# Kernel optimization log

Measured on AMD Instinct MI355X. Metric: run time of the kernel, lower is better.

Reference implementation:

```python
import jax, jax.numpy as jnp
import numpy as np

L1 = 0.05
L2 = 0.05
L3 = 0.05
L4 = 0.05
D_MIN = 1.0
EPS = 1e-12


def _pairwise_dist(x, y):
    sq = (jnp.sum(x * x, axis=-1)[:, None]
          + jnp.sum(y * y, axis=-1)[None, :]
          - 2.0 * (x @ y.T))
    return jnp.sqrt(jnp.clip(sq, EPS))


def setup_inputs() -> dict:
    key = jax.random.key(0)
    k1, k2, k3, k4, k5, k6 = jax.random.split(key, 6)
    B, C, D, d, P = 32768, 100, 1024, 512, 128
    return {
        "predictions": jax.random.normal(k1, (B, C), dtype=jnp.float32),
        "reconstructions": jax.random.normal(k2, (B, D), dtype=jnp.float32),
        "data": jax.random.normal(k3, (B, D), dtype=jnp.float32),
        "embeddings": jax.random.normal(k4, (B, d), dtype=jnp.float32),
        "prototypes": jax.random.normal(k5, (P, d), dtype=jnp.float32),
        "labels": jax.random.randint(k6, (B,), 0, C, dtype=jnp.int64),
    }


def reference(predictions, reconstructions, data, embeddings, prototypes, labels):
    B = predictions.shape[0]
    P = prototypes.shape[0]

    # Cross-entropy (mean reduction, class-index targets)
    logp = jax.nn.log_softmax(predictions, axis=-1)
    classification_loss = -jnp.mean(logp[jnp.arange(B), labels])

    # MSE reconstruction loss (mean reduction)
    reconstruction_loss = jnp.mean((reconstructions - data) ** 2)

    # Prototype diversity penalty: sum_{j<k} max(0, d_min - ||p_j - p_k||)^2
    proto_dist = _pairwise_dist(prototypes, prototypes)  # [P, P]
    hinge = jnp.maximum(0.0, D_MIN - proto_dist) ** 2
    upper = jnp.triu(jnp.ones((P, P), dtype=bool), k=1)
    diversity_penalty = jnp.sum(jnp.where(upper, hinge, 0.0))

    # Embedding-to-prototype distances [B, P], shared by similarity/coverage penalties
    dist = _pairwise_dist(embeddings, prototypes)
    similarity_penalty = jnp.sum(jnp.min(dist, axis=0)) / P
    coverage_penalty = jnp.sum(jnp.min(dist, axis=1)) / B

    total_loss = (classification_loss
                  + L1 * reconstruction_loss
                  + L2 * diversity_penalty
                  + L3 * similarity_penalty
                  + L4 * coverage_penalty)
    return total_loss
```

## Files before the change

### kernel.cpp

```cpp
#include <hip/hip_runtime.h>
#include <hip/hip_bf16.h>


constexpr float FEPS = 1e-12f;
constexpr float DMIN = 1.0f;

#define NB_DIST 512
#define NB_MSE  1024
#define NB_CE   256
#define NB_DIV  128

typedef unsigned short ushort_t;
typedef __attribute__((ext_vector_type(8))) short bf16x8;
typedef __attribute__((ext_vector_type(8))) unsigned short u16x8;
typedef __attribute__((ext_vector_type(4))) unsigned short u16x4;
typedef __attribute__((ext_vector_type(16))) float f32x16;
typedef __attribute__((ext_vector_type(4))) float f32x4;

__device__ __forceinline__ unsigned short f2b(float f) {
    unsigned u = __float_as_uint(f);
    u += 0x7FFFu + ((u >> 16) & 1u);
    return (unsigned short)(u >> 16);
}

union SmemU {
    struct {
        char     As[8192];
        char     Bs[16384];
        float    rown[64];
        float    pn[128];
        unsigned rowmin[64];
        unsigned colmin[128];
    } dist;
    struct { float pp[512]; float spp; float sred[4]; } div;
    struct { float sred[4]; } red;
};

__global__ __launch_bounds__(128) void conv_kernel(const float* __restrict__ proto,
                                                   ushort_t* __restrict__ pB,
                                                   float* __restrict__ pnorm,
                                                   float* __restrict__ ws,
                                                   unsigned* __restrict__ proto_min) {
    int p = blockIdx.x, q = threadIdx.x;
    if (q == 0) proto_min[p] = 0x7F7F7F7Fu;
    if (p == 0 && q < 4) ws[q] = 0.f;
    float4 v = ((const float4*)(proto + (size_t)p * 512))[q];
    u16x4 o = { f2b(v.x), f2b(v.y), f2b(v.z), f2b(v.w) };
    *(u16x4*)(pB + (size_t)p * 512 + q * 4) = o;
    float s = v.x * v.x + v.y * v.y + v.z * v.z + v.w * v.w;
    #pragma unroll
    for (int off = 32; off; off >>= 1) s += __shfl_xor(s, off);
    __shared__ float sr[2];
    if ((q & 63) == 0) sr[q >> 6] = s;
    __syncthreads();
    if (q == 0) pnorm[p] = sr[0] + sr[1];
}

template<bool PRECONV>
__device__ __forceinline__ void dist_body(SmemU& sm, int bid,
                                          const float* __restrict__ emb,
                                          const float* __restrict__ proto,
                                          const ushort_t* __restrict__ pB,
                                          const float* __restrict__ pnormG,
                                          unsigned* __restrict__ proto_min,
                                          float* __restrict__ cov_out) {
    char*     AsB     = sm.dist.As;
    char*     BsB     = sm.dist.Bs;
    float*    rownL   = sm.dist.rown;
    float*    pnL     = sm.dist.pn;
    unsigned* rowminL = sm.dist.rowmin;
    unsigned* colminL = sm.dist.colmin;

    const int t  = threadIdx.x;
    const int m0 = bid * 64;

    if (t < 64)  { rownL[t] = 0.f; rowminL[t] = 0x7F7F7F7Fu; }
    if (t < 128) { colminL[t] = 0x7F7F7F7Fu; pnL[t] = PRECONV ? pnormG[t] : 0.f; }
    __syncthreads();

    const int ra = t >> 2, qa = t & 3;
    const int pb = t >> 1, hb = t & 1;
    const int raz = ra & 7, pbz = pb & 7;

    const float4* aG  = (const float4*)(emb + (size_t)(m0 + ra) * 512 + qa * 16);
    const u16x8*  bG  = (const u16x8*)(pB) + (size_t)pb * 64 + hb * 4;
    const float4* bGf = (const float4*)(proto + (size_t)pb * 512 + hb * 32);

    const int lane = t & 63, wv = t >> 6;
    const int wr = wv >> 1, wc = wv & 1;
    const int lo = lane & 31, hi = lane >> 5;
    const int arow = wr * 32 + lo;
    const int arz  = arow & 7;
    const int p0 = wc * 64 + lo, p1 = p0 + 32;
    const int pz = p0 & 7;

    float4 av0 = aG[0], av1 = aG[1], av2 = aG[2], av3 = aG[3];
    u16x8  bv0, bv1, bv2, bv3;
    float4 bf0, bf1, bf2, bf3, bf4, bf5, bf6, bf7;
    if constexpr (PRECONV) { bv0 = bG[0]; bv1 = bG[1]; bv2 = bG[2]; bv3 = bG[3]; }
    else { bf0 = bGf[0]; bf1 = bGf[1]; bf2 = bGf[2]; bf3 = bGf[3];
           bf4 = bGf[4]; bf5 = bGf[5]; bf6 = bGf[6]; bf7 = bGf[7]; }

    f32x16 acc0 = {}, acc1 = {};

    char* Aw = AsB + ra * 128;
    char* Bw = BsB + pb * 128;
    const char* Ar  = AsB + arow * 128;
    const char* Br0 = BsB + p0 * 128;
    const char* Br1 = BsB + p1 * 128;

    for (int c = 0; c < 8; ++c) {
        {
            float nx = 0.f;
            nx = fmaf(av0.x, av0.x, nx); nx = fmaf(av0.y, av0.y, nx);
            nx = fmaf(av0.z, av0.z, nx); nx = fmaf(av0.w, av0.w, nx);
            nx = fmaf(av1.x, av1.x, nx); nx = fmaf(av1.y, av1.y, nx);
            nx = fmaf(av1.z, av1.z, nx); nx = fmaf(av1.w, av1.w, nx);
            nx = fmaf(av2.x, av2.x, nx); nx = fmaf(av2.y, av2.y, nx);
            nx = fmaf(av2.z, av2.z, nx); nx = fmaf(av2.w, av2.w, nx);
            nx = fmaf(av3.x, av3.x, nx); nx = fmaf(av3.y, av3.y, nx);
            nx = fmaf(av3.z, av3.z, nx); nx = fmaf(av3.w, av3.w, nx);
            atomicAdd(&rownL[ra], nx);
            u16x8 w0 = { f2b(av0.x), f2b(av0.y), f2b(av0.z), f2b(av0.w),
                         f2b(av1.x), f2b(av1.y), f2b(av1.z), f2b(av1.w) };
            u16x8 w1 = { f2b(av2.x), f2b(av2.y), f2b(av2.z), f2b(av2.w),
                         f2b(av3.x), f2b(av3.y), f2b(av3.z), f2b(av3.w) };
            *(u16x8*)(Aw + (((qa * 2 + 0) ^ raz) << 4)) = w0;
            *(u16x8*)(Aw + (((qa * 2 + 1) ^ raz) << 4)) = w1;

            if constexpr (PRECONV) {
                *(u16x8*)(Bw + (((hb * 4 + 0) ^ pbz) << 4)) = bv0;
                *(u16x8*)(Bw + (((hb * 4 + 1) ^ pbz) << 4)) = bv1;
                *(u16x8*)(Bw + (((hb * 4 + 2) ^ pbz) << 4)) = bv2;
                *(u16x8*)(Bw + (((hb * 4 + 3) ^ pbz) << 4)) = bv3;
            } else {
                float pns = 0.f;
                pns = fmaf(bf0.x, bf0.x, pns); pns = fmaf(bf0.y, bf0.y, pns);
                pns = fmaf(bf0.z, bf0.z, pns); pns = fmaf(bf0.w, bf0.w, pns);
                pns = fmaf(bf1.x, bf1.x, pns); pns = fmaf(bf1.y, bf1.y, pns);
                pns = fmaf(bf1.z, bf1.z, pns); pns = fmaf(bf1.w, bf1.w, pns);
                pns = fmaf(bf2.x, bf2.x, pns); pns = fmaf(bf2.y, bf2.y, pns);
                pns = fmaf(bf2.z, bf2.z, pns); pns = fmaf(bf2.w, bf2.w, pns);
                pns = fmaf(bf3.x, bf3.x, pns); pns = fmaf(bf3.y, bf3.y, pns);
                pns = fmaf(bf3.z, bf3.z, pns); pns = fmaf(bf3.w, bf3.w, pns);
                pns = fmaf(bf4.x, bf4.x, pns); pns = fmaf(bf4.y, bf4.y, pns);
                pns = fmaf(bf4.z, bf4.z, pns); pns = fmaf(bf4.w, bf4.w, pns);
                pns = fmaf(bf5.x, bf5.x, pns); pns = fmaf(bf5.y, bf5.y, pns);
                pns = fmaf(bf5.z, bf5.z, pns); pns = fmaf(bf5.w, bf5.w, pns);
                pns = fmaf(bf6.x, bf6.x, pns); pns = fmaf(bf6.y, bf6.y, pns);
                pns = fmaf(bf6.z, bf6.z, pns); pns = fmaf(bf6.w, bf6.w, pns);
                pns = fmaf(bf7.x, bf7.x, pns); pns = fmaf(bf7.y, bf7.y, pns);
                pns = fmaf(bf7.z, bf7.z, pns); pns = fmaf(bf7.w, bf7.w, pns);
                atomicAdd(&pnL[pb], pns);
                u16x8 x0 = { f2b(bf0.x), f2b(bf0.y), f2b(bf0.z), f2b(bf0.w),
                             f2b(bf1.x), f2b(bf1.y), f2b(bf1.z), f2b(bf1.w) };
                u16x8 x1 = { f2b(bf2.x), f2b(bf2.y), f2b(bf2.z), f2b(bf2.w),
                             f2b(bf3.x), f2b(bf3.y), f2b(bf3.z), f2b(bf3.w) };
                u16x8 x2 = { f2b(bf4.x), f2b(bf4.y), f2b(bf4.z), f2b(bf4.w),
                             f2b(bf5.x), f2b(bf5.y), f2b(bf5.z), f2b(bf5.w) };
                u16x8 x3 = { f2b(bf6.x), f2b(bf6.y), f2b(bf6.z), f2b(bf6.w),
                             f2b(bf7.x), f2b(bf7.y), f2b(bf7.z), f2b(bf7.w) };
                *(u16x8*)(Bw + (((hb * 4 + 0) ^ pbz) << 4)) = x0;
                *(u16x8*)(Bw + (((hb * 4 + 1) ^ pbz) << 4)) = x1;
                *(u16x8*)(Bw + (((hb * 4 + 2) ^ pbz) << 4)) = x2;
                *(u16x8*)(Bw + (((hb * 4 + 3) ^ pbz) << 4)) = x3;
            }
        }
        __syncthreads();
        if (c < 7) {
            av0 = aG[(c + 1) * 16 + 0]; av1 = aG[(c + 1) * 16 + 1];
            av2 = aG[(c + 1) * 16 + 2]; av3 = aG[(c + 1) * 16 + 3];
            if constexpr (PRECONV) {
                bv0 = bG[(c + 1) * 8 + 0]; bv1 = bG[(c + 1) * 8 + 1];
                bv2 = bG[(c + 1) * 8 + 2]; bv3 = bG[(c + 1) * 8 + 3];
            } else {
                bf0 = bGf[(c + 1) * 16 + 0]; bf1 = bGf[(c + 1) * 16 + 1];
                bf2 = bGf[(c + 1) * 16 + 2]; bf3 = bGf[(c + 1) * 16 + 3];
                bf4 = bGf[(c + 1) * 16 + 4]; bf5 = bGf[(c + 1) * 16 + 5];
                bf6 = bGf[(c + 1) * 16 + 6]; bf7 = bGf[(c + 1) * 16 + 7];
            }
        }
        #pragma unroll
        for (int s = 0; s < 4; ++s) {
            const int g = (s * 2 + hi);
            bf16x8 af = *(const bf16x8*)(Ar  + ((g ^ arz) << 4));
            bf16x8 b0 = *(const bf16x8*)(Br0 + ((g ^ pz)  << 4));
            bf16x8 b1 = *(const bf16x8*)(Br1 + ((g ^ pz)  << 4));
            acc0 = __builtin_amdgcn_mfma_f32_32x32x16_bf16(af, b0, acc0, 0, 0, 0);
            acc1 = __builtin_amdgcn_mfma_f32_32x32x16_bf16(af, b1, acc1, 0, 0, 0);
        }
        __syncthreads();
    }

    const float pn0 = pnL[p0], pn1 = pnL[p1];
    float cmin0 = 3.0e38f, cmin1 = 3.0e38f;
    #pragma unroll
    for (int r = 0; r < 16; ++r) {
        const int row = wr * 32 + (r & 3) + 8 * (r >> 2) + 4 * hi;
        const float nx = rownL[row];
        float d0 = sqrtf(fmaxf(nx + pn0 - 2.f * acc0[r], FEPS));
        float d1 = sqrtf(fmaxf(nx + pn1 - 2.f * acc1[r], FEPS));
        cmin0 = fminf(cmin0, d0);
        cmin1 = fminf(cmin1, d1);
        atomicMin(&rowminL[row], __float_as_uint(fminf(d0, d1)));
    }
    atomicMin(&colminL[p0], __float_as_uint(cmin0));
    atomicMin(&colminL[p1], __float_as_uint(cmin1));
    __syncthreads();

    if (t < 64) {
        float cv = __uint_as_float(rowminL[t]);
        #pragma unroll
        for (int o = 32; o; o >>= 1) cv += __shfl_xor(cv, o);
        if (t == 0) atomicAdd(cov_out, cv);
    }
    if (t < 128) atomicMin(&proto_min[t], colminL[t]);
}

__device__ __forceinline__ void mse_body(SmemU& sm, int mb,
                                         const float4* __restrict__ r,
                                         const float4* __restrict__ d,
                                         float* __restrict__ out, int n4) {
    const int t  = threadIdx.x;
    const int CH = (n4 + NB_MSE - 1) / NB_MSE;
    const int base = mb * CH;
    const int L = (base + CH <= n4) ? CH : (n4 - base);
    const f32x4* rb = (const f32x4*)(r + base);
    const f32x4* db = (const f32x4*)(d + base);
    float acc0 = 0.f, acc1 = 0.f, acc2 = 0.f, acc3 = 0.f;
    int k = t;
    for (; k + 7 * 256 < L; k += 8 * 256) {
        f32x4 a0 = __builtin_nontemporal_load(&rb[k + 0 * 256]);
        f32x4 a1 = __builtin_nontemporal_load(&rb[k + 1 * 256]);
        f32x4 a2 = __builtin_nontemporal_load(&rb[k + 2 * 256]);
        f32x4 a3 = __builtin_nontemporal_load(&rb[k + 3 * 256]);
        f32x4 a4 = __builtin_nontemporal_load(&rb[k + 4 * 256]);
        f32x4 a5 = __builtin_nontemporal_load(&rb[k + 5 * 256]);
        f32x4 a6 = __builtin_nontemporal_load(&rb[k + 6 * 256]);
        f32x4 a7 = __builtin_nontemporal_load(&rb[k + 7 * 256]);
        f32x4 b0 = __builtin_nontemporal_load(&db[k + 0 * 256]);
        f32x4 b1 = __builtin_nontemporal_load(&db[k + 1 * 256]);
        f32x4 b2 = __builtin_nontemporal_load(&db[k + 2 * 256]);
        f32x4 b3 = __builtin_nontemporal_load(&db[k + 3 * 256]);
        f32x4 b4 = __builtin_nontemporal_load(&db[k + 4 * 256]);
        f32x4 b5 = __builtin_nontemporal_load(&db[k + 5 * 256]);
        f32x4 b6 = __builtin_nontemporal_load(&db[k + 6 * 256]);
        f32x4 b7 = __builtin_nontemporal_load(&db[k + 7 * 256]);
        f32x4 e;
        e = a0 - b0; acc0 = fmaf(e.x, e.x, acc0); acc1 = fmaf(e.y, e.y, acc1);
                     acc2 = fmaf(e.z, e.z, acc2); acc3 = fmaf(e.w, e.w, acc3);
        e = a1 - b1; acc0 = fmaf(e.x, e.x, acc0); acc1 = fmaf(e.y, e.y, acc1);
                     acc2 = fmaf(e.z, e.z, acc2); acc3 = fmaf(e.w, e.w, acc3);
        e = a2 - b2; acc0 = fmaf(e.x, e.x, acc0); acc1 = fmaf(e.y, e.y, acc1);
                     acc2 = fmaf(e.z, e.z, acc2); acc3 = fmaf(e.w, e.w, acc3);
        e = a3 - b3; acc0 = fmaf(e.x, e.x, acc0); acc1 = fmaf(e.y, e.y, acc1);
                     acc2 = fmaf(e.z, e.z, acc2); acc3 = fmaf(e.w, e.w, acc3);
        e = a4 - b4; acc0 = fmaf(e.x, e.x, acc0); acc1 = fmaf(e.y, e.y, acc1);
                     acc2 = fmaf(e.z, e.z, acc2); acc3 = fmaf(e.w, e.w, acc3);
        e = a5 - b5; acc0 = fmaf(e.x, e.x, acc0); acc1 = fmaf(e.y, e.y, acc1);
                     acc2 = fmaf(e.z, e.z, acc2); acc3 = fmaf(e.w, e.w, acc3);
        e = a6 - b6; acc0 = fmaf(e.x, e.x, acc0); acc1 = fmaf(e.y, e.y, acc1);
                     acc2 = fmaf(e.z, e.z, acc2); acc3 = fmaf(e.w, e.w, acc3);
        e = a7 - b7; acc0 = fmaf(e.x, e.x, acc0); acc1 = fmaf(e.y, e.y, acc1);
                     acc2 = fmaf(e.z, e.z, acc2); acc3 = fmaf(e.w, e.w, acc3);
    }
    for (; k < L; k += 256) {
        f32x4 a = __builtin_nontemporal_load(&rb[k]);
        f32x4 b = __builtin_nontemporal_load(&db[k]);
        f32x4 e = a - b;
        acc0 = fmaf(e.x, e.x, acc0); acc1 = fmaf(e.y, e.y, acc1);
        acc2 = fmaf(e.z, e.z, acc2); acc3 = fmaf(e.w, e.w, acc3);
    }
    float acc = (acc0 + acc1) + (acc2 + acc3);
    #pragma unroll
    for (int o = 32; o; o >>= 1) acc += __shfl_xor(acc, o);
    int lane = t & 63, w = t >> 6;
    if (lane == 0) sm.red.sred[w] = acc;
    __syncthreads();
    if (t == 0) atomicAdd(out, sm.red.sred[0] + sm.red.sred[1]
                             + sm.red.sred[2] + sm.red.sred[3]);
}

__device__ __forceinline__ void ce_body(SmemU& sm, int cb,
                                        const float* __restrict__ pred,
                                        const int* __restrict__ lab,
                                        float* __restrict__ ce_out,
                                        int B, int C) {
    const int rows_per_wave = B / (NB_CE * 4);
    int lane = threadIdx.x & 63;
    int w    = threadIdx.x >> 6;
    int wid  = cb * 4 + w;
    float acc = 0.f;
    for (int i = 0; i < rows_per_wave; ++i) {
        int row = wid * rows_per_wave + i;
        const float* p = pred + (size_t)row * C;
        float v1 = (lane < C)      ? p[lane]      : -3.0e38f;
        float v2 = (lane + 64 < C) ? p[lane + 64] : -3.0e38f;
        float m = fmaxf(v1, v2);
        #pragma unroll
        for (int o = 32; o; o >>= 1) m = fmaxf(m, __shfl_xor(m, o));
        float s = ((lane < C) ? __expf(v1 - m) : 0.f)
                + ((lane + 64 < C) ? __expf(v2 - m) : 0.f);
        #pragma unroll
        for (int o = 32; o; o >>= 1) s += __shfl_xor(s, o);
        float lv = p[lab[row]];
        acc += m + __logf(s) - lv;
    }
    if (lane == 0) sm.red.sred[w] = acc;
    __syncthreads();
    if (threadIdx.x == 0) atomicAdd(ce_out, sm.red.sred[0] + sm.red.sred[1]
                                          + sm.red.sred[2] + sm.red.sred[3]);
}

__device__ __forceinline__ void div_body(SmemU& sm, int p,
                                         const float* __restrict__ proto,
                                         float* __restrict__ div_out, int dd) {
    int q = threadIdx.x;
    bool act = q < 128;
    if (act) for (int k = q; k < dd; k += 128) sm.div.pp[k] = proto[(size_t)p * dd + k];
    __syncthreads();
    float dot = 0.f, qq = 0.f;
    if (act) {
        const float4* pq4 = (const float4*)(proto + (size_t)q * dd);
        const float4* pp4 = (const float4*)sm.div.pp;
        for (int k4 = 0; k4 < dd / 4; ++k4) {
            float4 v = pq4[k4];
            float4 u = pp4[k4];
            dot = fmaf(u.x, v.x, dot); dot = fmaf(u.y, v.y, dot);
            dot = fmaf(u.z, v.z, dot); dot = fmaf(u.w, v.w, dot);
            qq  = fmaf(v.x, v.x, qq);  qq  = fmaf(v.y, v.y, qq);
            qq  = fmaf(v.z, v.z, qq);  qq  = fmaf(v.w, v.w, qq);
        }
        if (q == p) sm.div.spp = qq;
    }
    __syncthreads();
    float h2 = 0.f;
    if (act && q > p) {
        float sq = sm.div.spp + qq - 2.f * dot;
        float dist = sqrtf(fmaxf(sq, FEPS));
        float h = fmaxf(0.f, DMIN - dist);
        h2 = h * h;
    }
    #pragma unroll
    for (int o = 32; o; o >>= 1) h2 += __shfl_xor(h2, o);
    if ((q & 63) == 0) sm.div.sred[q >> 6] = h2;
    __syncthreads();
    if (q == 0) atomicAdd(div_out, sm.div.sred[0] + sm.div.sred[1]
                                 + sm.div.sred[2] + sm.div.sred[3]);
}

template<bool PRECONV>
__global__ __launch_bounds__(256) void fused_kernel(
        const float* __restrict__ pred, const int* __restrict__ lab,
        const float4* __restrict__ recon4, const float4* __restrict__ data4,
        const float* __restrict__ emb, const float* __restrict__ proto,
        const ushort_t* __restrict__ pB, const float* __restrict__ pnormG,
        float* __restrict__ ws, unsigned* __restrict__ proto_min,
        int B, int C, int n4, int dd) {
    __shared__ __attribute__((aligned(16))) SmemU sm;
    int bid = blockIdx.x;
    if (bid < NB_DIST) {
        dist_body<PRECONV>(sm, bid, emb, proto, pB, pnormG, proto_min, ws + 3);
    } else if (bid < NB_DIST + NB_MSE) {
        mse_body(sm, bid - NB_DIST, recon4, data4, ws + 1, n4);
    } else if (bid < NB_DIST + NB_MSE + NB_CE) {
        ce_body(sm, bid - NB_DIST - NB_MSE, pred, lab, ws + 0, B, C);
    } else {
        div_body(sm, bid - NB_DIST - NB_MSE - NB_CE, proto, ws + 2, dd);
    }
}

__global__ void final_kernel(const float* __restrict__ ws,
                             const unsigned* __restrict__ pmin,
                             float* __restrict__ out, int B, int D, int P) {
    float sim = 0.f;
    for (int i = 0; i < P; ++i) sim += __uint_as_float(pmin[i]);
    float ce  = ws[0] / (float)B;
    float mse = ws[1] / ((float)B * (float)D);
    out[0] = ce + 0.05f * mse + 0.05f * ws[2] + 0.05f * (sim / (float)P)
           + 0.05f * (ws[3] / (float)B);
}

extern "C" void kernel_launch(void* const* d_in, const int* in_sizes, int n_in,
                              void* d_out, int out_size, void* d_ws, size_t ws_size,
                              hipStream_t stream) {
    const float* pred  = (const float*)d_in[0];
    const float* recon = (const float*)d_in[1];
    const float* data  = (const float*)d_in[2];
    const float* emb   = (const float*)d_in[3];
    const float* proto = (const float*)d_in[4];
    const int*   lab   = (const int*)d_in[5];
    float* out = (float*)d_out;

    int B  = in_sizes[5];
    int C  = in_sizes[0] / B;
    int D  = in_sizes[1] / B;
    int dd = in_sizes[3] / B;
    int P  = in_sizes[4] / dd;

    float* ws = (float*)d_ws;
    unsigned* proto_min = (unsigned*)(ws + 4);
    float*    pnorm     = ws + 132;
    ushort_t* pB        = (ushort_t*)((char*)d_ws + 1280);
    bool preconv = ws_size >= (size_t)(1280 + 128 * 512 * 2);

    int n4 = (B * D) / 4;
    int grid = NB_DIST + NB_MSE + NB_CE + NB_DIV;
    if (preconv) {
        conv_kernel<<<128, 128, 0, stream>>>(proto, pB, pnorm, ws, proto_min);
        fused_kernel<true><<<grid, 256, 0, stream>>>(
            pred, lab, (const float4*)recon, (const float4*)data, emb, proto,
            pB, pnorm, ws, proto_min, B, C, n4, dd);
    } else {
        hipMemsetAsync(ws, 0, 4 * sizeof(float), stream);
        hipMemsetAsync(ws + 4, 0x7F, P * sizeof(unsigned), stream);
        fused_kernel<false><<<grid, 256, 0, stream>>>(
            pred, lab, (const float4*)recon, (const float4*)data, emb, proto,
            nullptr, nullptr, ws, proto_min, B, C, n4, dd);
    }
    final_kernel<<<1, 1, 0, stream>>>(ws, proto_min, out, B, D, P);
}
```

Baseline: 105.9 us.

## Pipeline distance GEMM with direct global-to-LDS prototype loads and register double-buffering

The preconverted distance path now loads bf16 prototype tiles straight into LDS with global_load_lds, pre-swizzling the source addresses. Embedding loads are double-buffered in registers with the next chunk prefetched before the current one is converted. Row-norm atomics are collapsed to one per thread at the end, and explicit waitcnt and barriers replace __syncthreads. Launch bounds now request 4 blocks per CU. This aims to hide memory latency and remove the register round-trip for B, at the risk of fragile hand-written waitcnt ordering and extra register pressure.

```diff
diff --git a/kernel.cpp b/kernel.cpp
--- a/kernel.cpp
+++ b/kernel.cpp
@@ -16,6 +16,9 @@
 typedef __attribute__((ext_vector_type(4))) unsigned short u16x4;
 typedef __attribute__((ext_vector_type(16))) float f32x16;
 typedef __attribute__((ext_vector_type(4))) float f32x4;
+
+typedef __attribute__((address_space(1))) const void gvoid_t;
+typedef __attribute__((address_space(3))) void lvoid_t;
 
 __device__ __forceinline__ unsigned short f2b(float f) {
     unsigned u = __float_as_uint(f);
@@ -56,14 +59,12 @@
     if (q == 0) pnorm[p] = sr[0] + sr[1];
 }
 
-template<bool PRECONV>
-__device__ __forceinline__ void dist_body(SmemU& sm, int bid,
-                                          const float* __restrict__ emb,
-                                          const float* __restrict__ proto,
-                                          const ushort_t* __restrict__ pB,
-                                          const float* __restrict__ pnormG,
-                                          unsigned* __restrict__ proto_min,
-                                          float* __restrict__ cov_out) {
+__device__ __forceinline__ void dist_body_fast(SmemU& sm, int bid,
+                                               const float* __restrict__ emb,
+                                               const ushort_t* __restrict__ pB,
+                                               const float* __restrict__ pnormG,
+                                               unsigned* __restrict__ proto_min,
+                                               float* __restrict__ cov_out) {
     char*     AsB     = sm.dist.As;
     char*     BsB     = sm.dist.Bs;
     float*    rownL   = sm.dist.rown;
@@ -75,16 +76,28 @@
     const int m0 = bid * 64;
 
     if (t < 64)  { rownL[t] = 0.f; rowminL[t] = 0x7F7F7F7Fu; }
-    if (t < 128) { colminL[t] = 0x7F7F7F7Fu; pnL[t] = PRECONV ? pnormG[t] : 0.f; }
-    __syncthreads();
-
-    const int ra = t >> 2, qa = t & 3;
-    const int pb = t >> 1, hb = t & 1;
-    const int raz = ra & 7, pbz = pb & 7;
-
-    const float4* aG  = (const float4*)(emb + (size_t)(m0 + ra) * 512 + qa * 16);
-    const u16x8*  bG  = (const u16x8*)(pB) + (size_t)pb * 64 + hb * 4;
-    const float4* bGf = (const float4*)(proto + (size_t)pb * 512 + hb * 32);
+    if (t < 128) { colminL[t] = 0x7F7F7F7Fu; pnL[t] = pnormG[t]; }
+
+    int aidx[4], rowi[4], swzi[4];
+    const float4* embF4 = (const float4*)emb;
+    #pragma unroll
+    for (int i = 0; i < 4; ++i) {
+        int flat = i * 256 + t;
+        int row = flat >> 4, colq = flat & 15;
+        rowi[i] = row;
+        aidx[i] = (m0 + row) * 128 + colq;
+        swzi[i] = row * 128 + ((((colq >> 1) ^ (row & 7)) << 4) | ((colq & 1) << 3));
+    }
+
+    const ushort_t* bsrcp[4];
+    char* bdstW[4];
+    #pragma unroll
+    for (int i = 0; i < 4; ++i) {
+        int f = i * 256 + t;
+        int pr = f >> 3, gb = f & 7;
+        bsrcp[i] = pB + pr * 512 + ((gb ^ (pr & 7)) << 3);
+        bdstW[i] = BsB + (size_t)(i * 256 + (t & ~63)) * 16;
+    }
 
     const int lane = t & 63, wv = t >> 6;
     const int wr = wv >> 1, wc = wv & 1;
@@ -93,16 +106,146 @@
     const int arz  = arow & 7;
     const int p0 = wc * 64 + lo, p1 = p0 + 32;
     const int pz = p0 & 7;
+    const char* Ar  = AsB + arow * 128;
+    const char* Br0 = BsB + p0 * 128;
+    const char* Br1 = BsB + p1 * 128;
+
+    float4 aE0 = embF4[aidx[0]], aE1 = embF4[aidx[1]],
+           aE2 = embF4[aidx[2]], aE3 = embF4[aidx[3]];
+    float4 aO0, aO1, aO2, aO3;
+    float rn0 = 0.f, rn1 = 0.f, rn2 = 0.f, rn3 = 0.f;
+    f32x16 acc0 = {}, acc1 = {};
+    __syncthreads();
+
+#define DIST_CHUNK(c, W0, W1, W2, W3, L0, L1, L2, L3)                          \
+    {                                                                          \
+        const int kc = (c) * 64;                                               \
+        __builtin_amdgcn_global_load_lds((gvoid_t*)(bsrcp[0] + kc),            \
+                                         (lvoid_t*)bdstW[0], 16, 0, 0);        \
+        __builtin_amdgcn_global_load_lds((gvoid_t*)(bsrcp[1] + kc),            \
+                                         (lvoid_t*)bdstW[1], 16, 0, 0);        \
+        __builtin_amdgcn_global_load_lds((gvoid_t*)(bsrcp[2] + kc),            \
+                                         (lvoid_t*)bdstW[2], 16, 0, 0);        \
+        __builtin_amdgcn_global_load_lds((gvoid_t*)(bsrcp[3] + kc),            \
+                                         (lvoid_t*)bdstW[3], 16, 0, 0);        \
+        __builtin_amdgcn_sched_barrier(0);                                     \
+        {                                                                      \
+            const int kn = ((c) < 7 ? (c) + 1 : 7) * 16;                       \
+            L0 = embF4[aidx[0] + kn]; L1 = embF4[aidx[1] + kn];                \
+            L2 = embF4[aidx[2] + kn]; L3 = embF4[aidx[3] + kn];                \
+        }                                                                      \
+        __builtin_amdgcn_sched_barrier(0);                                     \
+        rn0 = fmaf(W0.x, W0.x, rn0); rn0 = fmaf(W0.y, W0.y, rn0);              \
+        rn0 = fmaf(W0.z, W0.z, rn0); rn0 = fmaf(W0.w, W0.w, rn0);              \
+        rn1 = fmaf(W1.x, W1.x, rn1); rn1 = fmaf(W1.y, W1.y, rn1);              \
+        rn1 = fmaf(W1.z, W1.z, rn1); rn1 = fmaf(W1.w, W1.w, rn1);              \
+        rn2 = fmaf(W2.x, W2.x, rn2); rn2 = fmaf(W2.y, W2.y, rn2);              \
+        rn2 = fmaf(W2.z, W2.z, rn2); rn2 = fmaf(W2.w, W2.w, rn2);              \
+        rn3 = fmaf(W3.x, W3.x, rn3); rn3 = fmaf(W3.y, W3.y, rn3);              \
+        rn3 = fmaf(W3.z, W3.z, rn3); rn3 = fmaf(W3.w, W3.w, rn3);              \
+        { u16x4 u = { f2b(W0.x), f2b(W0.y), f2b(W0.z), f2b(W0.w) };            \
+          *(u16x4*)(AsB + swzi[0]) = u; }                                      \
+        { u16x4 u = { f2b(W1.x), f2b(W1.y), f2b(W1.z), f2b(W1.w) };            \
+          *(u16x4*)(AsB + swzi[1]) = u; }                                      \
+        { u16x4 u = { f2b(W2.x), f2b(W2.y), f2b(W2.z), f2b(W2.w) };            \
+          *(u16x4*)(AsB + swzi[2]) = u; }                                      \
+        { u16x4 u = { f2b(W3.x), f2b(W3.y), f2b(W3.z), f2b(W3.w) };            \
+          *(u16x4*)(AsB + swzi[3]) = u; }                                      \
+        asm volatile("s_waitcnt vmcnt(4)" ::: "memory");                       \
+        asm volatile("s_waitcnt lgkmcnt(0)" ::: "memory");                     \
+        __builtin_amdgcn_s_barrier();                                          \
+        __builtin_amdgcn_sched_barrier(0);                                     \
+        _Pragma("unroll")                                                      \
+        for (int s = 0; s < 4; ++s) {                                          \
+            const int g = (s * 2 + hi);                                        \
+            bf16x8 af = *(const bf16x8*)(Ar  + ((g ^ arz) << 4));              \
+            bf16x8 b0 = *(const bf16x8*)(Br0 + ((g ^ pz)  << 4));              \
+            bf16x8 b1 = *(const bf16x8*)(Br1 + ((g ^ pz)  << 4));              \
+            acc0 = __builtin_amdgcn_mfma_f32_32x32x16_bf16(af, b0, acc0, 0,0,0); \
+            acc1 = __builtin_amdgcn_mfma_f32_32x32x16_bf16(af, b1, acc1, 0,0,0); \
+        }                                                                      \
+        asm volatile("s_waitcnt lgkmcnt(0)" ::: "memory");                     \
+        __builtin_amdgcn_s_barrier();                                          \
+        __builtin_amdgcn_sched_barrier(0);                                     \
+    }
+
+    #pragma unroll
+    for (int c = 0; c < 8; c += 2) {
+        DIST_CHUNK(c,     aE0, aE1, aE2, aE3, aO0, aO1, aO2, aO3)
+        DIST_CHUNK(c + 1, aO0, aO1, aO2, aO3, aE0, aE1, aE2, aE3)
+    }
+#undef DIST_CHUNK
+
+    atomicAdd(&rownL[rowi[0]], rn0);
+    atomicAdd(&rownL[rowi[1]], rn1);
+    atomicAdd(&rownL[rowi[2]], rn2);
+    atomicAdd(&rownL[rowi[3]], rn3);
+    __syncthreads();
+
+    const float pn0 = pnL[p0], pn1 = pnL[p1];
+    float cmin0 = 3.0e38f, cmin1 = 3.0e38f;
+    #pragma unroll
+    for (int r = 0; r < 16; ++r) {
+        const int row = wr * 32 + (r & 3) + 8 * (r >> 2) + 4 * hi;
+        const float nx = rownL[row];
+        float d0 = sqrtf(fmaxf(nx + pn0 - 2.f * acc0[r], FEPS));
+        float d1 = sqrtf(fmaxf(nx + pn1 - 2.f * acc1[r], FEPS));
+        cmin0 = fminf(cmin0, d0);
+        cmin1 = fminf(cmin1, d1);
+        atomicMin(&rowminL[row], __float_as_uint(fminf(d0, d1)));
+    }
+    atomicMin(&colminL[p0], __float_as_uint(cmin0));
+    atomicMin(&colminL[p1], __float_as_uint(cmin1));
+    __syncthreads();
+
+    if (t < 64) {
+        float cv = __uint_as_float(rowminL[t]);
+        #pragma unroll
+        for (int o = 32; o; o >>= 1) cv += __shfl_xor(cv, o);
+        if (t == 0) atomicAdd(cov_out, cv);
+    }
+    if (t < 128) atomicMin(&proto_min[t], colminL[t]);
+}
+
+__device__ __forceinline__ void dist_body_slow(SmemU& sm, int bid,
+                                               const float* __restrict__ emb,
+                                               const float* __restrict__ proto,
+                                               unsigned* __restrict__ proto_min,
+                                               float* __restrict__ cov_out) {
+    char*     AsB     = sm.dist.As;
+    char*     BsB     = sm.dist.Bs;
+    float*    rownL   = sm.dist.rown;
+    float*    pnL     = sm.dist.pn;
+    unsigned* rowminL = sm.dist.rowmin;
+    unsigned* colminL = sm.dist.colmin;
+
+    const int t  = threadIdx.x;
+    const int m0 = bid * 64;
+
+    if (t < 64)  { rownL[t] = 0.f; rowminL[t] = 0x7F7F7F7Fu; }
+    if (t < 128) { colminL[t] = 0x7F7F7F7Fu; pnL[t] = 0.f; }
+    __syncthreads();
+
+    const int ra = t >> 2, qa = t & 3;
+    const int pb = t >> 1, hb = t & 1;
+    const int raz = ra & 7, pbz = pb & 7;
+
+    const float4* aG  = (const float4*)(emb + (size_t)(m0 + ra) * 512 + qa * 16);
+    const float4* bGf = (const float4*)(proto + (size_t)pb * 512 + hb * 32);
+
+    const int lane = t & 63, wv = t >> 6;
+    const int wr = wv >> 1, wc = wv & 1;
+    const int lo = lane & 31, hi = lane >> 5;
+    const int arow = wr * 32 + lo;
+    const int arz  = arow & 7;
+    const int p0 = wc * 64 + lo, p1 = p0 + 32;
+    const int pz = p0 & 7;
 
     float4 av0 = aG[0], av1 = aG[1], av2 = aG[2], av3 = aG[3];
-    u16x8  bv0, bv1, bv2, bv3;
-    float4 bf0, bf1, bf2, bf3, bf4, bf5, bf6, bf7;
-    if constexpr (PRECONV) { bv0 = bG[0]; bv1 = bG[1]; bv2 = bG[2]; bv3 = bG[3]; }
-    else { bf0 = bGf[0]; bf1 = bGf[1]; bf2 = bGf[2]; bf3 = bGf[3];
-           bf4 = bGf[4]; bf5 = bGf[5]; bf6 = bGf[6]; bf7 = bGf[7]; }
+    float4 bf0 = bGf[0], bf1 = bGf[1], bf2 = bGf[2], bf3 = bGf[3],
+           bf4 = bGf[4], bf5 = bGf[5], bf6 = bGf[6], bf7 = bGf[7];
 
     f32x16 acc0 = {}, acc1 = {};
-
     char* Aw = AsB + ra * 128;
     char* Bw = BsB + pb * 128;
     const char* Ar  = AsB + arow * 128;
@@ -128,57 +271,45 @@
             *(u16x8*)(Aw + (((qa * 2 + 0) ^ raz) << 4)) = w0;
             *(u16x8*)(Aw + (((qa * 2 + 1) ^ raz) << 4)) = w1;
 
-            if constexpr (PRECONV) {
-                *(u16x8*)(Bw + (((hb * 4 + 0) ^ pbz) << 4)) = bv0;
-                *(u16x8*)(Bw + (((hb * 4 + 1) ^ pbz) << 4)) = bv1;
-                *(u16x8*)(Bw + (((hb * 4 + 2) ^ pbz) << 4)) = bv2;
-                *(u16x8*)(Bw + (((hb * 4 + 3) ^ pbz) << 4)) = bv3;
-            } else {
-                float pns = 0.f;
-                pns = fmaf(bf0.x, bf0.x, pns); pns = fmaf(bf0.y, bf0.y, pns);
-                pns = fmaf(bf0.z, bf0.z, pns); pns = fmaf(bf0.w, bf0.w, pns);
-                pns = fmaf(bf1.x, bf1.x, pns); pns = fmaf(bf1.y, bf1.y, pns);
-                pns = fmaf(bf1.z, bf1.z, pns); pns = fmaf(bf1.w, bf1.w, pns);
-                pns = fmaf(bf2.x, bf2.x, pns); pns = fmaf(bf2.y, bf2.y, pns);
-                pns = fmaf(bf2.z, bf2.z, pns); pns = fmaf(bf2.w, bf2.w, pns);
-                pns = fmaf(bf3.x, bf3.x, pns); pns = fmaf(bf3.y, bf3.y, pns);
-                pns = fmaf(bf3.z, bf3.z, pns); pns = fmaf(bf3.w, bf3.w, pns);
-                pns = fmaf(bf4.x, bf4.x, pns); pns = fmaf(bf4.y, bf4.y, pns);
-                pns = fmaf(bf4.z, bf4.z, pns); pns = fmaf(bf4.w, bf4.w, pns);
-                pns = fmaf(bf5.x, bf5.x, pns); pns = fmaf(bf5.y, bf5.y, pns);
-                pns = fmaf(bf5.z, bf5.z, pns); pns = fmaf(bf5.w, bf5.w, pns);
-                pns = fmaf(bf6.x, bf6.x, pns); pns = fmaf(bf6.y, bf6.y, pns);
-                pns = fmaf(bf6.z, bf6.z, pns); pns = fmaf(bf6.w, bf6.w, pns);
-                pns = fmaf(bf7.x, bf7.x, pns); pns = fmaf(bf7.y, bf7.y, pns);
-                pns = fmaf(bf7.z, bf7.z, pns); pns = fmaf(bf7.w, bf7.w, pns);
-                atomicAdd(&pnL[pb], pns);
-                u16x8 x0 = { f2b(bf0.x), f2b(bf0.y), f2b(bf0.z), f2b(bf0.w),
-                             f2b(bf1.x), f2b(bf1.y), f2b(bf1.z), f2b(bf1.w) };
-                u16x8 x1 = { f2b(bf2.x), f2b(bf2.y), f2b(bf2.z), f2b(bf2.w),
-                             f2b(bf3.x), f2b(bf3.y), f2b(bf3.z), f2b(bf3.w) };
-                u16x8 x2 = { f2b(bf4.x), f2b(bf4.y), f2b(bf4.z), f2b(bf4.w),
-                             f2b(bf5.x), f2b(bf5.y), f2b(bf5.z), f2b(bf5.w) };
-                u16x8 x3 = { f2b(bf6.x), f2b(bf6.y), f2b(bf6.z), f2b(bf6.w),
-                             f2b(bf7.x), f2b(bf7.y), f2b(bf7.z), f2b(bf7.w) };
-                *(u16x8*)(Bw + (((hb * 4 + 0) ^ pbz) << 4)) = x0;
-                *(u16x8*)(Bw + (((hb * 4 + 1) ^ pbz) << 4)) = x1;
-                *(u16x8*)(Bw + (((hb * 4 + 2) ^ pbz) << 4)) = x2;
-                *(u16x8*)(Bw + (((hb * 4 + 3) ^ pbz) << 4)) = x3;
-            }
+            float pns = 0.f;
+            pns = fmaf(bf0.x, bf0.x, pns); pns = fmaf(bf0.y, bf0.y, pns);
+            pns = fmaf(bf0.z, bf0.z, pns); pns = fmaf(bf0.w, bf0.w, pns);
+            pns = fmaf(bf1.x, bf1.x, pns); pns = fmaf(bf1.y, bf1.y, pns);
+            pns = fmaf(bf1.z, bf1.z, pns); pns = fmaf(bf1.w, bf1.w, pns);
+            pns = fmaf(bf2.x, bf2.x, pns); pns = fmaf(bf2.y, bf2.y, pns);
+            pns = fmaf(bf2.z, bf2.z, pns); pns = fmaf(bf2.w, bf2.w, pns);
+            pns = fmaf(bf3.x, bf3.x, pns); pns = fmaf(bf3.y, bf3.y, pns);
+            pns = fmaf(bf3.z, bf3.z, pns); pns = fmaf(bf3.w, bf3.w, pns);
+            pns = fmaf(bf4.x, bf4.x, pns); pns = fmaf(bf4.y, bf4.y, pns);
+            pns = fmaf(bf4.z, bf4.z, pns); pns = fmaf(bf4.w, bf4.w, pns);
+            pns = fmaf(bf5.x, bf5.x, pns); pns = fmaf(bf5.y, bf5.y, pns);
+            pns = fmaf(bf5.z, bf5.z, pns); pns = fmaf(bf5.w, bf5.w, pns);
+            pns = fmaf(bf6.x, bf6.x, pns); pns = fmaf(bf6.y, bf6.y, pns);
+            pns = fmaf(bf6.z, bf6.z, pns); pns = fmaf(bf6.w, bf6.w, pns);
+            pns = fmaf(bf7.x, bf7.x, pns); pns = fmaf(bf7.y, bf7.y, pns);
+            pns = fmaf(bf7.z, bf7.z, pns); pns = fmaf(bf7.w, bf7.w, pns);
+            atomicAdd(&pnL[pb], pns);
+            u16x8 x0 = { f2b(bf0.x), f2b(bf0.y), f2b(bf0.z), f2b(bf0.w),
+                         f2b(bf1.x), f2b(bf1.y), f2b(bf1.z), f2b(bf1.w) };
+            u16x8 x1 = { f2b(bf2.x), f2b(bf2.y), f2b(bf2.z), f2b(bf2.w),
+                         f2b(bf3.x), f2b(bf3.y), f2b(bf3.z), f2b(bf3.w) };
+            u16x8 x2 = { f2b(bf4.x), f2b(bf4.y), f2b(bf4.z), f2b(bf4.w),
+                         f2b(bf5.x), f2b(bf5.y), f2b(bf5.z), f2b(bf5.w) };
+            u16x8 x3 = { f2b(bf6.x), f2b(bf6.y), f2b(bf6.z), f2b(bf6.w),
+                         f2b(bf7.x), f2b(bf7.y), f2b(bf7.z), f2b(bf7.w) };
+            *(u16x8*)(Bw + (((hb * 4 + 0) ^ pbz) << 4)) = x0;
+            *(u16x8*)(Bw + (((hb * 4 + 1) ^ pbz) << 4)) = x1;
+            *(u16x8*)(Bw + (((hb * 4 + 2) ^ pbz) << 4)) = x2;
+            *(u16x8*)(Bw + (((hb * 4 + 3) ^ pbz) << 4)) = x3;
         }
         __syncthreads();
         if (c < 7) {
             av0 = aG[(c + 1) * 16 + 0]; av1 = aG[(c + 1) * 16 + 1];
             av2 = aG[(c + 1) * 16 + 2]; av3 = aG[(c + 1) * 16 + 3];
-            if constexpr (PRECONV) {
-                bv0 = bG[(c + 1) * 8 + 0]; bv1 = bG[(c + 1) * 8 + 1];
-                bv2 = bG[(c + 1) * 8 + 2]; bv3 = bG[(c + 1) * 8 + 3];
-            } else {
-                bf0 = bGf[(c + 1) * 16 + 0]; bf1 = bGf[(c + 1) * 16 + 1];
-                bf2 = bGf[(c + 1) * 16 + 2]; bf3 = bGf[(c + 1) * 16 + 3];
-                bf4 = bGf[(c + 1) * 16 + 4]; bf5 = bGf[(c + 1) * 16 + 5];
-                bf6 = bGf[(c + 1) * 16 + 6]; bf7 = bGf[(c + 1) * 16 + 7];
-            }
+            bf0 = bGf[(c + 1) * 16 + 0]; bf1 = bGf[(c + 1) * 16 + 1];
+            bf2 = bGf[(c + 1) * 16 + 2]; bf3 = bGf[(c + 1) * 16 + 3];
+            bf4 = bGf[(c + 1) * 16 + 4]; bf5 = bGf[(c + 1) * 16 + 5];
+            bf6 = bGf[(c + 1) * 16 + 6]; bf7 = bGf[(c + 1) * 16 + 7];
         }
         #pragma unroll
         for (int s = 0; s < 4; ++s) {
@@ -350,7 +481,7 @@
 }
 
 template<bool PRECONV>
-__global__ __launch_bounds__(256) void fused_kernel(
+__global__ __launch_bounds__(256, 4) void fused_kernel(
         const float* __restrict__ pred, const int* __restrict__ lab,
         const float4* __restrict__ recon4, const float4* __restrict__ data4,
         const float* __restrict__ emb, const float* __restrict__ proto,
@@ -360,7 +491,10 @@
     __shared__ __attribute__((aligned(16))) SmemU sm;
     int bid = blockIdx.x;
     if (bid < NB_DIST) {
-        dist_body<PRECONV>(sm, bid, emb, proto, pB, pnormG, proto_min, ws + 3);
+        if constexpr (PRECONV)
+            dist_body_fast(sm, bid, emb, pB, pnormG, proto_min, ws + 3);
+        else
+            dist_body_slow(sm, bid, emb, proto, proto_min, ws + 3);
     } else if (bid < NB_DIST + NB_MSE) {
         mse_body(sm, bid - NB_DIST, recon4, data4, ws + 1, n4);
     } else if (bid < NB_DIST + NB_MSE + NB_CE) {
```

Result: no change. 104.1 us (-1.7%).
